# Kernel tuning notes

Measured on AMD Instinct MI355X. Metric: run time of the kernel, lower is better.

Reference implementation:

```python
import jax, jax.numpy as jnp
import numpy as np

BLOCK = 64
EPS = 1e-6
N_HEADS = 16


def _rope(t, cos, sin):
    # t: (B,S,H,hd); cos/sin: (S, hd//2) -> broadcast (1,S,1,hd//2)
    B, S, H, hd = t.shape
    tr = t.reshape(B, S, H, hd // 2, 2)
    t0, t1 = tr[..., 0], tr[..., 1]
    c = cos[None, :, None, :]
    s = sin[None, :, None, :]
    o0 = t0 * c - t1 * s
    o1 = t0 * s + t1 * c
    return jnp.stack([o0, o1], axis=-1).reshape(B, S, H, hd)


def setup_inputs() -> dict:
    key = jax.random.key(0)
    ks = jax.random.split(key, 6)
    B, S, D = 1, 2048, 2048
    hd = D // N_HEADS
    x = jax.random.normal(ks[0], (B, S, D), dtype=jnp.float32)
    # rotary table: theta_i = 10000^(-2i/hd)
    inv_freq = 1.0 / (10000.0 ** (jnp.arange(0, hd, 2, dtype=jnp.float32) / hd))
    t = jnp.arange(S, dtype=jnp.float32)
    freqs = jnp.outer(t, inv_freq)  # (S, hd//2)
    freqs_cos = jnp.cos(freqs)
    freqs_sin = jnp.sin(freqs)
    std = 0.02
    Wq = jax.random.normal(ks[1], (D, D), dtype=jnp.float32) * std
    Wk = jax.random.normal(ks[2], (D, D), dtype=jnp.float32) * std
    Wv = jax.random.normal(ks[3], (D, D), dtype=jnp.float32) * std
    Wo = jax.random.normal(ks[4], (D, D), dtype=jnp.float32) * std
    mask = jnp.ones((1, 1), dtype=bool)  # non-None mask => no masking in original code
    return {"x": x, "freqs_cos": freqs_cos, "freqs_sin": freqs_sin,
            "Wq": Wq, "Wk": Wk, "Wv": Wv, "Wo": Wo, "mask": mask}


def reference(x, freqs_cos, freqs_sin, Wq, Wk, Wv, Wo, mask):
    B, S, D = x.shape
    H = N_HEADS
    hd = D // H
    scale = hd ** -0.5
    nb = S // BLOCK

    q = (x @ Wq.T).reshape(B, S, H, hd)
    k = (x @ Wk.T).reshape(B, S, H, hd)
    v = (x @ Wv.T).reshape(B, S, H, hd)
    q = _rope(q, freqs_cos, freqs_sin)
    k = _rope(k, freqs_cos, freqs_sin)

    # block views: (B, nb, BLOCK, H, hd)
    qb = q.reshape(B, nb, BLOCK, H, hd)
    kb = k.reshape(B, nb, BLOCK, H, hd)
    vb = v.reshape(B, nb, BLOCK, H, hd)

    # per-(i,j) block scores: (B, nb_i, nb_j, H, BLOCK_q, BLOCK_k)
    s = jnp.einsum('binhd,bjmhd->bijhnm', qb, kb) * scale
    # NOTE: original module (mask is not None path) applies NO causal mask and
    # uses the per-block local max (no running-max rescale) -- reproduced exactly.
    m = jnp.max(s, axis=-1, keepdims=True)
    p = jnp.exp(s - m)
    # denominator: sum of per-block row sums over all j blocks -> (B, nb, H, BLOCK)
    L = p.sum(axis=-1).sum(axis=2)
    # numerator: sum over j blocks of p @ v -> (B, nb, BLOCK, H, hd)
    O = jnp.einsum('bijhnm,bjmhd->binhd', p, vb).reshape(B, S, H, hd)
    Lr = L.transpose(0, 1, 3, 2).reshape(B, S, H, 1)  # (B,S,H,1)
    O = O / (Lr + EPS)
    return O.reshape(B, S, D) @ Wo.T
```

## Files before the change

### kernel.cpp

```cpp
#include <hip/hip_runtime.h>
#include <hip/hip_bf16.h>
#include <math.h>

#define SEQ 2048
#define DM  2048
#define NH  16
#define HD  128
#define SCALE 0.08838834764831845f

typedef __bf16 bf16_t;
typedef __bf16 bf16x8 __attribute__((ext_vector_type(8)));
typedef __bf16 bf16x4 __attribute__((ext_vector_type(4)));
typedef float  f32x4  __attribute__((ext_vector_type(4)));
typedef int    i32x4  __attribute__((ext_vector_type(4)));

typedef const __attribute__((address_space(1))) void* gas_ptr;
typedef __attribute__((address_space(3))) void* las_ptr;

__device__ __forceinline__ void gload_lds16(const void* g, void* l) {
    __builtin_amdgcn_global_load_lds((gas_ptr)g, (las_ptr)l, 16, 0, 0);
}

__device__ __forceinline__ f32x4 mfma_bf16(bf16x8 a, bf16x8 b, f32x4 c) {
    return __builtin_amdgcn_mfma_f32_16x16x32_bf16(a, b, c, 0, 0, 0);
}

__device__ __forceinline__ unsigned cvtpk_bf16(float lo, float hi) {
    unsigned d;
    asm("v_cvt_pk_bf16_f32 %0, %1, %2" : "=v"(d) : "v"(lo), "v"(hi));
    return d;
}

__device__ __forceinline__ bf16x8 read_frag64(const bf16_t* lds, int row, int k) {
    int chunk = (k >> 3) ^ (row & 7);
    return *(const bf16x8*)(lds + row * 64 + chunk * 8);
}
__device__ __forceinline__ bf16x8 read_frag128(const bf16_t* lds, int row, int k) {
    int chunk = k >> 3;
    chunk = (chunk & 8) | ((chunk ^ row) & 7);
    return *(const bf16x8*)(lds + row * 128 + chunk * 8);
}
__device__ __forceinline__ bf16x8 read_frag32(const bf16_t* lds, int row, int k) {
    int L = row >> 1;
    int u = ((row & 1) << 2) | (k >> 3);
    int c = u ^ (L & 7);
    return *(const bf16x8*)(lds + ((L << 3) + c) * 8);
}

__global__ __launch_bounds__(256) void cvt5(
    const float* __restrict__ s0, const float* __restrict__ s1,
    const float* __restrict__ s2, const float* __restrict__ s3,
    const float* __restrict__ s4,
    bf16_t* __restrict__ d0, bf16_t* __restrict__ d1, bf16_t* __restrict__ d2,
    bf16_t* __restrict__ d3, bf16_t* __restrict__ d4)
{
    int which = blockIdx.y;
    const float* s; bf16_t* d;
    switch (which) {
        case 0: s = s0; d = d0; break;
        case 1: s = s1; d = d1; break;
        case 2: s = s2; d = d2; break;
        case 3: s = s3; d = d3; break;
        default: s = s4; d = d4; break;
    }
    size_t idx = ((size_t)blockIdx.x * 256 + threadIdx.x) * 4;
    float4 v = *(const float4*)(s + idx);
    bf16x4 o = { (bf16_t)v.x, (bf16_t)v.y, (bf16_t)v.z, (bf16_t)v.w };
    *(bf16x4*)(d + idx) = o;
}

__global__ __launch_bounds__(512, 2) void qkv_pipe(
    const bf16_t* __restrict__ A,
    const bf16_t* __restrict__ B0, const bf16_t* __restrict__ B1,
    const bf16_t* __restrict__ B2,
    bf16_t* __restrict__ Oq, bf16_t* __restrict__ Ok, bf16_t* __restrict__ Ov,
    const float* __restrict__ fcos, const float* __restrict__ fsin)
{
    __shared__ bf16_t lds3[49152];

    const int tid = threadIdx.x;
    const int lane = tid & 63;
    const int w = tid >> 6;
    const int wm = w >> 2;
    const int wn = w & 3;
    const int g = lane >> 4, r15 = lane & 15;

    const int bm = blockIdx.x;
    const int bny = blockIdx.y;
    const int sel = bny >> 3;
    const int bnl = bny & 7;
    const bf16_t* Bp = (sel == 0) ? B0 : (sel == 1) ? B1 : B2;

    const size_t arow0 = (size_t)bm * 256;
    const size_t brow0 = (size_t)bnl * 256;

    int ci0 = tid, ci1 = 512 + tid;
    int L0 = ci0 >> 3, u0 = (ci0 & 7) ^ (L0 & 7);
    int L1 = ci1 >> 3, u1 = (ci1 & 7) ^ (L1 & 7);
    int mrow0 = (L0 << 1) | (u0 >> 2), kc0 = u0 & 3;
    int mrow1 = (L1 << 1) | (u1 >> 2), kc1 = u1 & 3;
    const bf16_t* gA0 = A  + (arow0 + mrow0) * DM + kc0 * 8;
    const bf16_t* gA1 = A  + (arow0 + mrow1) * DM + kc1 * 8;
    const bf16_t* gB0 = Bp + (brow0 + mrow0) * DM + kc0 * 8;
    const bf16_t* gB1 = Bp + (brow0 + mrow1) * DM + kc1 * 8;
    const int dst0 = (0 * 512 + w * 64) * 16;
    const int dst1 = (1 * 512 + w * 64) * 16;

    const int NT = DM / 32;

    f32x4 acc[8][4] = {};

    {
        char* s0a = (char*)(lds3);
        char* s0b = (char*)(lds3 + 8192);
        char* s1a = (char*)(lds3 + 16384);
        char* s1b = (char*)(lds3 + 16384 + 8192);
        gload_lds16(gA0 + 0 * 32, s0a + dst0);
        gload_lds16(gB0 + 0 * 32, s0b + dst0);
        gload_lds16(gA1 + 0 * 32, s0a + dst1);
        gload_lds16(gB1 + 0 * 32, s0b + dst1);
        gload_lds16(gA0 + 1 * 32, s1a + dst0);
        gload_lds16(gB0 + 1 * 32, s1b + dst0);
        gload_lds16(gA1 + 1 * 32, s1a + dst1);
        gload_lds16(gB1 + 1 * 32, s1b + dst1);
    }
    asm volatile("s_waitcnt vmcnt(4)" ::: "memory");
    __builtin_amdgcn_s_barrier();

    int sk = 0, sp = 2;
    for (int k = 0; k < NT; ++k) {
        const bf16_t* sA = lds3 + sk * 16384;
        const bf16_t* sB = sA + 8192;
        char* pA = (char*)(lds3 + sp * 16384);
        char* pB = pA + 8192 * 2;
        const bool pf = (k + 2 < NT);
        const int kO = (k + 2) * 32;

        bf16x8 afrag[4], bfrag[4];
        #pragma unroll
        for (int m = 0; m < 4; ++m)
            afrag[m] = read_frag32(sA, wm * 128 + m * 16 + r15, g * 8);
        #pragma unroll
        for (int n = 0; n < 4; ++n)
            bfrag[n] = read_frag32(sB, wn * 64 + n * 16 + r15, g * 8);
        if (pf) {
            gload_lds16(gA0 + kO, pA + dst0);
            gload_lds16(gB0 + kO, pB + dst0);
        }
        __builtin_amdgcn_s_barrier();
        __builtin_amdgcn_s_setprio(1);
        #pragma unroll
        for (int m = 0; m < 4; ++m)
            #pragma unroll
            for (int n = 0; n < 4; ++n)
                acc[m][n] = mfma_bf16(afrag[m], bfrag[n], acc[m][n]);
        __builtin_amdgcn_s_setprio(0);
        __builtin_amdgcn_s_barrier();

        #pragma unroll
        for (int m = 0; m < 4; ++m)
            afrag[m] = read_frag32(sA, wm * 128 + (m + 4) * 16 + r15, g * 8);
        if (pf) {
            gload_lds16(gA1 + kO, pA + dst1);
            gload_lds16(gB1 + kO, pB + dst1);
        }
        if (k < NT - 2) asm volatile("s_waitcnt vmcnt(4)" ::: "memory");
        else            asm volatile("s_waitcnt vmcnt(0)" ::: "memory");
        __builtin_amdgcn_s_barrier();
        __builtin_amdgcn_s_setprio(1);
        #pragma unroll
        for (int m = 0; m < 4; ++m)
            #pragma unroll
            for (int n = 0; n < 4; ++n)
                acc[m + 4][n] = mfma_bf16(afrag[m], bfrag[n], acc[m + 4][n]);
        __builtin_amdgcn_s_setprio(0);
        __builtin_amdgcn_s_barrier();

        sk = (sk == 2) ? 0 : sk + 1;
        sp = (sp == 2) ? 0 : sp + 1;
    }

    const int r0 = bm * 256 + wm * 128;
    const int c0 = bnl * 256 + wn * 64;

    if (sel == 2) {
        #pragma unroll
        for (int m = 0; m < 8; ++m) {
            int rowb = r0 + m * 16 + g * 4;
            #pragma unroll
            for (int n = 0; n < 4; ++n) {
                int col = c0 + n * 16 + r15;
                bf16x4 pk = { (bf16_t)acc[m][n][0], (bf16_t)acc[m][n][1],
                              (bf16_t)acc[m][n][2], (bf16_t)acc[m][n][3] };
                *(bf16x4*)&Ov[(size_t)col * SEQ + rowb] = pk;
            }
        }
    } else {
        bf16_t* dst = (sel == 0) ? Oq : Ok;
        #pragma unroll
        for (int m = 0; m < 8; ++m) {
            int rowb = r0 + m * 16 + g * 4;
            #pragma unroll
            for (int n = 0; n < 4; ++n) {
                int col = c0 + n * 16 + r15;
                int f = (col & (HD - 1)) >> 1;
                float sgn = (col & 1) ? 1.0f : -1.0f;
                #pragma unroll
                for (int r = 0; r < 4; ++r) {
                    float mine = acc[m][n][r];
                    float other = __shfl_xor(mine, 1);
                    float cc = fcos[(rowb + r) * (HD / 2) + f];
                    float ss = fsin[(rowb + r) * (HD / 2) + f];
                    float o = mine * cc + sgn * other * ss;
                    dst[(size_t)(rowb + r) * DM + col] = (bf16_t)o;
                }
            }
        }
    }
}

__global__ __launch_bounds__(256) void gemm_fin(
    const bf16_t* __restrict__ A, const bf16_t* __restrict__ B0,
    float* __restrict__ Of)
{
    __shared__ bf16_t lA[128 * 64];
    __shared__ bf16_t lB[128 * 64];

    const int tid = threadIdx.x;
    const int lane = tid & 63;
    const int w = tid >> 6;
    const int wm = w >> 1, wn = w & 1;
    const int g = lane >> 4, r15 = lane & 15;

    const int bm = blockIdx.x;
    const int bn = blockIdx.y;

    f32x4 acc[4][4] = {};

    const size_t arow0 = (size_t)bm * 128;
    const size_t brow0 = (size_t)bn * 128;

    for (int kt = 0; kt < DM / 64; ++kt) {
        const int k0 = kt * 64;
        #pragma unroll
        for (int i = 0; i < 4; ++i) {
            int c = i * 256 + tid;
            int row = c >> 3;
            int ck = (c ^ row) & 7;
            const bf16_t* ga = A + (arow0 + row) * DM + k0 + ck * 8;
            gload_lds16(ga, (char*)lA + (i * 256 + w * 64) * 16);
            const bf16_t* gb = B0 + (brow0 + row) * DM + k0 + ck * 8;
            gload_lds16(gb, (char*)lB + (i * 256 + w * 64) * 16);
        }
        __syncthreads();
        #pragma unroll
        for (int kk = 0; kk < 2; ++kk) {
            bf16x8 af[4], bfr[4];
            #pragma unroll
            for (int m = 0; m < 4; ++m)
                af[m] = read_frag64(lA, wm * 64 + m * 16 + r15, kk * 32 + g * 8);
            #pragma unroll
            for (int n = 0; n < 4; ++n)
                bfr[n] = read_frag64(lB, wn * 64 + n * 16 + r15, kk * 32 + g * 8);
            #pragma unroll
            for (int m = 0; m < 4; ++m)
                #pragma unroll
                for (int n = 0; n < 4; ++n)
                    acc[m][n] = mfma_bf16(af[m], bfr[n], acc[m][n]);
        }
        __syncthreads();
    }

    const int r0 = bm * 128 + wm * 64;
    const int c0 = bn * 128 + wn * 64;
    #pragma unroll
    for (int m = 0; m < 4; ++m) {
        int rowb = r0 + m * 16 + g * 4;
        #pragma unroll
        for (int n = 0; n < 4; ++n) {
            int col = c0 + n * 16 + r15;
            #pragma unroll
            for (int r = 0; r < 4; ++r)
                Of[(size_t)(rowb + r) * DM + col] = acc[m][n][r];
        }
    }
}

__global__ __launch_bounds__(512, 2) void attn_k2(
    const bf16_t* __restrict__ Q, const bf16_t* __restrict__ Kb,
    const bf16_t* __restrict__ Vt, bf16_t* __restrict__ Ob)
{
    __shared__ bf16_t lk[2 * 64 * 128];
    __shared__ bf16_t lv[2 * 128 * 64];

    const int tid = threadIdx.x;
    const int lane = tid & 63;
    const int w = tid >> 6;
    const int g = lane >> 4, r15 = lane & 15;
    const int qb = blockIdx.x, h = blockIdx.y;

    const int lo = g & 1, hb = g >> 1;
    const int e_src = (lo << 5) + r15;
    const int o_src = e_src + 16;
    const int sA = hb ? o_src : e_src;
    const int sB = hb ? e_src : o_src;

    bf16x8 qf[4];
    {
        const bf16_t* qrow = Q + (size_t)(qb * 128 + w * 16 + r15) * DM + h * HD + g * 8;
        #pragma unroll
        for (int ks = 0; ks < 4; ++ks)
            qf[ks] = *(const bf16x8*)(qrow + ks * 32);
    }

    f32x4 oacc[8] = {};
    float Lsum = 0.f;

    #define STAGE_KV(JJ, BUF)                                                     \
    {                                                                             \
        _Pragma("unroll")                                                         \
        for (int i = 0; i < 2; ++i) {                                             \
            int c = i * 512 + tid;                                                \
            int row = c >> 4, ckl = c & 15;                                       \
            int ck = (ckl & 8) | ((ckl ^ row) & 7);                               \
            const bf16_t* gk = Kb + (size_t)((JJ) * 64 + row) * DM + h * HD + ck * 8; \
            gload_lds16(gk, (char*)lk + (BUF) * 16384 + (i * 512 + w * 64) * 16); \
        }                                                                         \
        _Pragma("unroll")                                                         \
        for (int i = 0; i < 2; ++i) {                                             \
            int c = i * 512 + tid;                                                \
            int row = c >> 3;                                                     \
            int ck = (c ^ row) & 7;                                               \
            const bf16_t* gv = Vt + (size_t)(h * HD + row) * SEQ + (JJ) * 64 + ck * 8; \
            gload_lds16(gv, (char*)lv + (BUF) * 16384 + (i * 512 + w * 64) * 16); \
        }                                                                         \
    }

    STAGE_KV(0, 0);
    asm volatile("s_waitcnt vmcnt(0)" ::: "memory");
    __builtin_amdgcn_s_barrier();

    for (int j = 0; j < SEQ / 64; ++j) {
        const int cur = j & 1;
        const bf16_t* lkc = lk + cur * 8192;
        const bf16_t* lvc = lv + cur * 8192;
        if (j < SEQ / 64 - 1) STAGE_KV(j + 1, cur ^ 1);

        f32x4 sacc[4] = {};
        __builtin_amdgcn_s_setprio(1);
        #pragma unroll
        for (int ks = 0; ks < 4; ++ks) {
            #pragma unroll
            for (int n = 0; n < 4; ++n) {
                bf16x8 kf = read_frag128(lkc, n * 16 + r15, ks * 32 + g * 8);
                sacc[n] = mfma_bf16(kf, qf[ks], sacc[n]);
            }
        }
        __builtin_amdgcn_s_setprio(0);

        float mx0 = fmaxf(fmaxf(sacc[0][0], sacc[0][1]), fmaxf(sacc[0][2], sacc[0][3]));
        float mx1 = fmaxf(fmaxf(sacc[1][0], sacc[1][1]), fmaxf(sacc[1][2], sacc[1][3]));
        float mx2 = fmaxf(fmaxf(sacc[2][0], sacc[2][1]), fmaxf(sacc[2][2], sacc[2][3]));
        float mx3 = fmaxf(fmaxf(sacc[3][0], sacc[3][1]), fmaxf(sacc[3][2], sacc[3][3]));
        float mx = fmaxf(fmaxf(mx0, mx1), fmaxf(mx2, mx3));
        mx = fmaxf(mx, __shfl_xor(mx, 16));
        mx = fmaxf(mx, __shfl_xor(mx, 32));

        float p[4][4];
        float ls = 0.f;
        #pragma unroll
        for (int n = 0; n < 4; ++n)
            #pragma unroll
            for (int r = 0; r < 4; ++r) {
                float pv = __expf((sacc[n][r] - mx) * SCALE);
                p[n][r] = pv;
                ls += pv;
            }
        Lsum += ls;

        unsigned D00 = cvtpk_bf16(p[0][0], p[0][1]), D01 = cvtpk_bf16(p[0][2], p[0][3]);
        unsigned D10 = cvtpk_bf16(p[1][0], p[1][1]), D11 = cvtpk_bf16(p[1][2], p[1][3]);
        unsigned D20 = cvtpk_bf16(p[2][0], p[2][1]), D21 = cvtpk_bf16(p[2][2], p[2][3]);
        unsigned D30 = cvtpk_bf16(p[3][0], p[3][1]), D31 = cvtpk_bf16(p[3][2], p[3][3]);

        unsigned r0 = __shfl((int)(lo ? D10 : D00), sA);
        unsigned r1 = __shfl((int)(lo ? D11 : D01), sA);
        unsigned r2 = __shfl((int)(lo ? D00 : D10), sB);
        unsigned r3 = __shfl((int)(lo ? D01 : D11), sB);
        unsigned r4 = __shfl((int)(lo ? D30 : D20), sA);
        unsigned r5 = __shfl((int)(lo ? D31 : D21), sA);
        unsigned r6 = __shfl((int)(lo ? D20 : D30), sB);
        unsigned r7 = __shfl((int)(lo ? D21 : D31), sB);
        i32x4 w0, w1;
        w0[0] = (int)(hb ? r2 : r0);  w0[1] = (int)(hb ? r3 : r1);
        w0[2] = (int)(hb ? r0 : r2);  w0[3] = (int)(hb ? r1 : r3);
        w1[0] = (int)(hb ? r6 : r4);  w1[1] = (int)(hb ? r7 : r5);
        w1[2] = (int)(hb ? r4 : r6);  w1[3] = (int)(hb ? r5 : r7);
        bf16x8 pa0 = __builtin_bit_cast(bf16x8, w0);
        bf16x8 pa1 = __builtin_bit_cast(bf16x8, w1);

        __builtin_amdgcn_s_setprio(1);
        #pragma unroll
        for (int n = 0; n < 8; ++n) {
            bf16x8 bv = read_frag64(lvc, n * 16 + r15, g * 8);
            oacc[n] = mfma_bf16(pa0, bv, oacc[n]);
        }
        #pragma unroll
        for (int n = 0; n < 8; ++n) {
            bf16x8 bv = read_frag64(lvc, n * 16 + r15, 32 + g * 8);
            oacc[n] = mfma_bf16(pa1, bv, oacc[n]);
        }
        __builtin_amdgcn_s_setprio(0);

        asm volatile("s_waitcnt vmcnt(0)" ::: "memory");
        __builtin_amdgcn_s_barrier();
    }

    float L = Lsum;
    L += __shfl_xor(L, 16);
    L += __shfl_xor(L, 32);
    float inv = 1.0f / (L + 1e-6f);
    float invr[4];
    #pragma unroll
    for (int r = 0; r < 4; ++r)
        invr[r] = __shfl(inv, g * 4 + r);

    #pragma unroll
    for (int n = 0; n < 8; ++n) {
        int col = h * HD + n * 16 + r15;
        int rowb = qb * 128 + w * 16 + g * 4;
        #pragma unroll
        for (int r = 0; r < 4; ++r)
            Ob[(size_t)(rowb + r) * DM + col] = (bf16_t)(oacc[n][r] * invr[r]);
    }
}

extern "C" void kernel_launch(void* const* d_in, const int* in_sizes, int n_in,
                              void* d_out, int out_size, void* d_ws, size_t ws_size,
                              hipStream_t stream)
{
    const float* x    = (const float*)d_in[0];
    const float* fcos = (const float*)d_in[1];
    const float* fsin = (const float*)d_in[2];
    const float* Wq   = (const float*)d_in[3];
    const float* Wk   = (const float*)d_in[4];
    const float* Wv   = (const float*)d_in[5];
    const float* Wo   = (const float*)d_in[6];
    float* out = (float*)d_out;

    const size_t NE = (size_t)DM * SEQ;
    bf16_t* ws  = (bf16_t*)d_ws;
    bf16_t* xb  = ws;
    bf16_t* wqb = ws + 1 * NE;
    bf16_t* wkb = ws + 2 * NE;
    bf16_t* wvb = ws + 3 * NE;
    bf16_t* wob = ws + 4 * NE;
    bf16_t* qr  = ws + 5 * NE;
    bf16_t* kr  = ws + 6 * NE;
    bf16_t* vt  = ws + 7 * NE;
    bf16_t* ob  = ws + 8 * NE;

    hipLaunchKernelGGL(cvt5, dim3(4096, 5), dim3(256), 0, stream,
                       x, Wq, Wk, Wv, Wo, xb, wqb, wkb, wvb, wob);

    hipLaunchKernelGGL(qkv_pipe, dim3(8, 24), dim3(512), 0, stream,
                       xb, wqb, wkb, wvb, qr, kr, vt, fcos, fsin);

    hipLaunchKernelGGL(attn_k2, dim3(16, 16), dim3(512), 0, stream,
                       qr, kr, vt, ob);

    hipLaunchKernelGGL(gemm_fin, dim3(16, 16), dim3(256), 0, stream,
                       ob, wob, out);
}
```

Measured before the change: 189.1 us.

## Restructure QKV GEMM pipeline into K=64 double-buffered slabs with new LDS swizzle

Rewrites the QKV projection GEMM main loop. It now stages K=64 tiles as separate A and B half-slabs in a 128KB LDS double buffer, uses a simpler XOR swizzle, and runs a fully unrolled schedule of eight phases per iteration. Each phase issues one stage of async global-to-LDS loads with finer vmcnt gating, aiming for deeper prefetch and fewer waits per MFMA. The cost is doubled LDS use (128KB per block), which with launch bounds of 2 blocks per CU may cut occupancy, and the hand-unrolled macro schedule is fragile.

```diff
diff --git a/kernel.cpp b/kernel.cpp
--- a/kernel.cpp
+++ b/kernel.cpp
@@ -40,11 +40,9 @@
     chunk = (chunk & 8) | ((chunk ^ row) & 7);
     return *(const bf16x8*)(lds + row * 128 + chunk * 8);
 }
-__device__ __forceinline__ bf16x8 read_frag32(const bf16_t* lds, int row, int k) {
-    int L = row >> 1;
-    int u = ((row & 1) << 2) | (k >> 3);
-    int c = u ^ (L & 7);
-    return *(const bf16x8*)(lds + ((L << 3) + c) * 8);
+__device__ __forceinline__ bf16x8 read_slab(const bf16_t* sl, int row, int g) {
+    int j = g ^ ((row >> 1) & 3);
+    return *(const bf16x8*)(sl + row * 32 + j * 8);
 }
 
 __global__ __launch_bounds__(256) void cvt5(
@@ -69,6 +67,12 @@
     *(bf16x4*)(d + idx) = o;
 }
 
+#define BARX() asm volatile("s_barrier" ::: "memory")
+#define VMW8 asm volatile("s_waitcnt vmcnt(8)" ::: "memory")
+#define VMW4 asm volatile("s_waitcnt vmcnt(4)" ::: "memory")
+#define VMW0 asm volatile("s_waitcnt vmcnt(0)" ::: "memory")
+#define NOGATE
+
 __global__ __launch_bounds__(512, 2) void qkv_pipe(
     const bf16_t* __restrict__ A,
     const bf16_t* __restrict__ B0, const bf16_t* __restrict__ B1,
@@ -76,14 +80,14 @@
     bf16_t* __restrict__ Oq, bf16_t* __restrict__ Ok, bf16_t* __restrict__ Ov,
     const float* __restrict__ fcos, const float* __restrict__ fsin)
 {
-    __shared__ bf16_t lds3[49152];
+    __shared__ bf16_t lds[65536];
 
     const int tid = threadIdx.x;
     const int lane = tid & 63;
     const int w = tid >> 6;
     const int wm = w >> 2;
     const int wn = w & 3;
-    const int g = lane >> 4, r15 = lane & 15;
+    const int g4 = lane >> 4, r15 = lane & 15;
 
     const int bm = blockIdx.x;
     const int bny = blockIdx.y;
@@ -94,91 +98,87 @@
     const size_t arow0 = (size_t)bm * 256;
     const size_t brow0 = (size_t)bnl * 256;
 
-    int ci0 = tid, ci1 = 512 + tid;
-    int L0 = ci0 >> 3, u0 = (ci0 & 7) ^ (L0 & 7);
-    int L1 = ci1 >> 3, u1 = (ci1 & 7) ^ (L1 & 7);
-    int mrow0 = (L0 << 1) | (u0 >> 2), kc0 = u0 & 3;
-    int mrow1 = (L1 << 1) | (u1 >> 2), kc1 = u1 & 3;
-    const bf16_t* gA0 = A  + (arow0 + mrow0) * DM + kc0 * 8;
-    const bf16_t* gA1 = A  + (arow0 + mrow1) * DM + kc1 * 8;
-    const bf16_t* gB0 = Bp + (brow0 + mrow0) * DM + kc0 * 8;
-    const bf16_t* gB1 = Bp + (brow0 + mrow1) * DM + kc1 * 8;
-    const int dst0 = (0 * 512 + w * 64) * 16;
-    const int dst1 = (1 * 512 + w * 64) * 16;
-
-    const int NT = DM / 32;
+    const int row0 = tid >> 2;
+    const int kj0  = (tid & 3) ^ ((row0 >> 1) & 3);
+    const bf16_t* pA = A  + (arow0 + row0) * DM + kj0 * 8;
+    const bf16_t* pB = Bp + (brow0 + row0) * DM + kj0 * 8;
+    char* ldsb = (char*)lds;
+    const int off0 = tid * 16;
+    const int off1 = 8192 + tid * 16;
+
+    #define STAGE_HT(S) do { if ((S) < 128) {                                   \
+        const int T_ = (S) >> 2, a_ = (S) & 3;                                  \
+        const int ko_ = T_ * 64 + ((a_ >> 1) << 5);                             \
+        char* dst_ = ldsb + (((T_ & 1) << 16) | ((a_ & 1) << 15) | ((a_ >> 1) << 14)); \
+        const bf16_t* s0_ = (a_ & 1) ? pB : pA;                                 \
+        gload_lds16(s0_ + ko_, dst_ + off0);                                    \
+        gload_lds16(s0_ + 128 * DM + ko_, dst_ + off1);                         \
+    } } while (0)
+
+    const bf16_t* b0A0 = lds;
+    const bf16_t* b0A1 = lds + 8192;
+    const bf16_t* b0B0 = lds + 16384;
+    const bf16_t* b0B1 = lds + 24576;
+    const bf16_t* b1A0 = lds + 32768;
+    const bf16_t* b1A1 = lds + 40960;
+    const bf16_t* b1B0 = lds + 49152;
+    const bf16_t* b1B1 = lds + 57344;
 
     f32x4 acc[8][4] = {};
 
+    #define PHASE(ASL, BSL, MH, SIDX, GATE, READB)                              \
+    {                                                                           \
+        _Pragma("unroll")                                                       \
+        for (int m = 0; m < 4; ++m)                                             \
+            af[m] = read_slab((ASL), wm * 128 + (MH) * 64 + m * 16 + r15, g4);  \
+        if (READB) {                                                            \
+            _Pragma("unroll")                                                   \
+            for (int n = 0; n < 4; ++n)                                         \
+                bfr[n] = read_slab((BSL), wn * 64 + n * 16 + r15, g4);          \
+        }                                                                       \
+        STAGE_HT(SIDX);                                                         \
+        GATE;                                                                   \
+        BARX();                                                                 \
+        __builtin_amdgcn_s_setprio(1);                                          \
+        _Pragma("unroll")                                                       \
+        for (int m = 0; m < 4; ++m)                                             \
+            _Pragma("unroll")                                                   \
+            for (int n = 0; n < 4; ++n)                                         \
+                acc[(MH) * 4 + m][n] = mfma_bf16(af[m], bfr[n], acc[(MH) * 4 + m][n]); \
+        __builtin_amdgcn_s_setprio(0);                                          \
+        BARX();                                                                 \
+    }
+
+    STAGE_HT(0); STAGE_HT(1); STAGE_HT(2); STAGE_HT(3); STAGE_HT(4); STAGE_HT(5);
+    VMW8;
+    BARX();
+
+    for (int i = 0; i < 15; ++i) {
+        const int s0 = 6 + i * 8;
+        bf16x8 af[4], bfr[4];
+        PHASE(b0A0, b0B0, 0, s0 + 0, NOGATE, 1)
+        PHASE(b0A0, b0B0, 1, s0 + 1, VMW8,   0)
+        PHASE(b0A1, b0B1, 0, s0 + 2, NOGATE, 1)
+        PHASE(b0A1, b0B1, 1, s0 + 3, VMW8,   0)
+        PHASE(b1A0, b1B0, 0, s0 + 4, NOGATE, 1)
+        PHASE(b1A0, b1B0, 1, s0 + 5, VMW8,   0)
+        PHASE(b1A1, b1B1, 0, s0 + 6, NOGATE, 1)
+        PHASE(b1A1, b1B1, 1, s0 + 7, VMW8,   0)
+    }
     {
-        char* s0a = (char*)(lds3);
-        char* s0b = (char*)(lds3 + 8192);
-        char* s1a = (char*)(lds3 + 16384);
-        char* s1b = (char*)(lds3 + 16384 + 8192);
-        gload_lds16(gA0 + 0 * 32, s0a + dst0);
-        gload_lds16(gB0 + 0 * 32, s0b + dst0);
-        gload_lds16(gA1 + 0 * 32, s0a + dst1);
-        gload_lds16(gB1 + 0 * 32, s0b + dst1);
-        gload_lds16(gA0 + 1 * 32, s1a + dst0);
-        gload_lds16(gB0 + 1 * 32, s1b + dst0);
-        gload_lds16(gA1 + 1 * 32, s1a + dst1);
-        gload_lds16(gB1 + 1 * 32, s1b + dst1);
-    }
-    asm volatile("s_waitcnt vmcnt(4)" ::: "memory");
-    __builtin_amdgcn_s_barrier();
-
-    int sk = 0, sp = 2;
-    for (int k = 0; k < NT; ++k) {
-        const bf16_t* sA = lds3 + sk * 16384;
-        const bf16_t* sB = sA + 8192;
-        char* pA = (char*)(lds3 + sp * 16384);
-        char* pB = pA + 8192 * 2;
-        const bool pf = (k + 2 < NT);
-        const int kO = (k + 2) * 32;
-
-        bf16x8 afrag[4], bfrag[4];
-        #pragma unroll
-        for (int m = 0; m < 4; ++m)
-            afrag[m] = read_frag32(sA, wm * 128 + m * 16 + r15, g * 8);
-        #pragma unroll
-        for (int n = 0; n < 4; ++n)
-            bfrag[n] = read_frag32(sB, wn * 64 + n * 16 + r15, g * 8);
-        if (pf) {
-            gload_lds16(gA0 + kO, pA + dst0);
-            gload_lds16(gB0 + kO, pB + dst0);
-        }
-        __builtin_amdgcn_s_barrier();
-        __builtin_amdgcn_s_setprio(1);
-        #pragma unroll
-        for (int m = 0; m < 4; ++m)
-            #pragma unroll
-            for (int n = 0; n < 4; ++n)
-                acc[m][n] = mfma_bf16(afrag[m], bfrag[n], acc[m][n]);
-        __builtin_amdgcn_s_setprio(0);
-        __builtin_amdgcn_s_barrier();
-
-        #pragma unroll
-        for (int m = 0; m < 4; ++m)
-            afrag[m] = read_frag32(sA, wm * 128 + (m + 4) * 16 + r15, g * 8);
-        if (pf) {
-            gload_lds16(gA1 + kO, pA + dst1);
-            gload_lds16(gB1 + kO, pB + dst1);
-        }
-        if (k < NT - 2) asm volatile("s_waitcnt vmcnt(4)" ::: "memory");
-        else            asm volatile("s_waitcnt vmcnt(0)" ::: "memory");
-        __builtin_amdgcn_s_barrier();
-        __builtin_amdgcn_s_setprio(1);
-        #pragma unroll
-        for (int m = 0; m < 4; ++m)
-            #pragma unroll
-            for (int n = 0; n < 4; ++n)
-                acc[m + 4][n] = mfma_bf16(afrag[m], bfrag[n], acc[m + 4][n]);
-        __builtin_amdgcn_s_setprio(0);
-        __builtin_amdgcn_s_barrier();
-
-        sk = (sk == 2) ? 0 : sk + 1;
-        sp = (sp == 2) ? 0 : sp + 1;
-    }
+        const int s0 = 6 + 15 * 8;
+        bf16x8 af[4], bfr[4];
+        PHASE(b0A0, b0B0, 0, s0 + 0, NOGATE, 1)
+        PHASE(b0A0, b0B0, 1, s0 + 1, VMW8,   0)
+        PHASE(b0A1, b0B1, 0, s0 + 2, NOGATE, 1)
+        PHASE(b0A1, b0B1, 1, s0 + 3, VMW4,   0)
+        PHASE(b1A0, b1B0, 0, s0 + 4, NOGATE, 1)
+        PHASE(b1A0, b1B0, 1, s0 + 5, VMW0,   0)
+        PHASE(b1A1, b1B1, 0, s0 + 6, NOGATE, 1)
+        PHASE(b1A1, b1B1, 1, s0 + 7, NOGATE, 0)
+    }
+    #undef PHASE
+    #undef STAGE_HT
 
     const int r0 = bm * 256 + wm * 128;
     const int c0 = bnl * 256 + wn * 64;
@@ -186,7 +186,7 @@
     if (sel == 2) {
         #pragma unroll
         for (int m = 0; m < 8; ++m) {
-            int rowb = r0 + m * 16 + g * 4;
+            int rowb = r0 + m * 16 + g4 * 4;
             #pragma unroll
             for (int n = 0; n < 4; ++n) {
                 int col = c0 + n * 16 + r15;
@@ -199,7 +199,7 @@
         bf16_t* dst = (sel == 0) ? Oq : Ok;
         #pragma unroll
         for (int m = 0; m < 8; ++m) {
-            int rowb = r0 + m * 16 + g * 4;
+            int rowb = r0 + m * 16 + g4 * 4;
             #pragma unroll
             for (int n = 0; n < 4; ++n) {
                 int col = c0 + n * 16 + r15;
```

After: 183.0 us. -3.2%, faster.
